# Kernel optimization log

Measured on AMD Instinct MI355X. Metric: run time of the kernel, lower is better.

Reference implementation:

```python
import jax, jax.numpy as jnp
import numpy as np

Z, Y, X = 16, 128, 128
B = 2
N_R, N_L = 12000, 20000   # active voxels per batch element (radar / lidar)
C = 64
IN_DIM = 4
NUM_LAYER = 2
K_LIST = (64, 32)         # knn fan-out = 64 / 2**layer
EPS = 1e-5


def _make_voxels(rng, n_per_batch):
    # unique voxel coords per batch, sorted by linear index (batch-major rows)
    out = []
    for b in range(B):
        lin = np.sort(rng.choice(Z * Y * X, size=n_per_batch, replace=False))
        z = lin // (Y * X); y = (lin // X) % Y; x = lin % X
        out.append(np.stack([np.full(n_per_batch, b), z, y, x], 1))
    return np.concatenate(out, 0).astype(np.int32)


def _nbr_map(coords):
    # 3x3x3 submanifold-conv rulebook: row index of each neighbor, -1 if absent
    b = coords[:, 0].astype(np.int64); z = coords[:, 1]; y = coords[:, 2]; x = coords[:, 3]
    keys = ((b * Z + z) * Y + y) * X + x  # globally sorted
    N = coords.shape[0]
    nbr = np.full((N, 27), -1, np.int64)
    k = 0
    for dz in (-1, 0, 1):
        for dy in (-1, 0, 1):
            for dx in (-1, 0, 1):
                nz, ny, nx = z + dz, y + dy, x + dx
                ok = (nz >= 0) & (nz < Z) & (ny >= 0) & (ny < Y) & (nx >= 0) & (nx < X)
                cand = ((b * Z + nz) * Y + ny) * X + nx
                pos = np.searchsorted(keys, cand)
                pos_c = np.clip(pos, 0, N - 1)
                hit = ok & (keys[pos_c] == cand)
                nbr[:, k] = np.where(hit, pos_c, -1)
                k += 1
    return nbr


def setup_inputs() -> dict:
    rng = np.random.default_rng(0)
    key = jax.random.key(0)
    ks = jax.random.split(key, 16)
    coordsR = _make_voxels(rng, N_R)
    coordsL = _make_voxels(rng, N_L)
    nbrR = _nbr_map(coordsR)
    nbrL = _nbr_map(coordsL)
    NLt = B * N_L
    # knn indices (global row ids into radar rows of same batch)
    knn0 = coordsL[:, 0:1].astype(np.int64) * N_R + rng.integers(0, N_R, (NLt, K_LIST[0]))
    knn1 = coordsL[:, 0:1].astype(np.int64) * N_R + rng.integers(0, N_R, (NLt, K_LIST[1]))
    sc = 1.0 / np.sqrt(27 * C).astype(np.float32)
    inp = {
        "featR": jax.random.normal(ks[0], (B * N_R, IN_DIM), jnp.float32),
        "featL": jax.random.normal(ks[1], (NLt, IN_DIM), jnp.float32),
        "img": jax.random.normal(ks[2], (B, 512), jnp.float32),
        "Win": jax.random.normal(ks[3], (2, IN_DIM, C), jnp.float32) * 0.1,
        "bin_": jnp.zeros((2, C), jnp.float32),
        # [layer, branch(R/L), conv(sp,subm_a,subm_b), 27, Cin, Cout]
        "Wconv": jax.random.normal(ks[4], (NUM_LAYER, 2, 3, 27, C, C), jnp.float32) * sc,
        "bconv": jnp.zeros((NUM_LAYER, 2, 3, C), jnp.float32),
        "bng": jnp.ones((NUM_LAYER, 2, 3, C), jnp.float32),
        "bnb": jnp.zeros((NUM_LAYER, 2, 3, C), jnp.float32),
        "Wimg": jax.random.normal(ks[5], (NUM_LAYER, 512, C), jnp.float32) * 0.05,
        "bimg": jnp.zeros((NUM_LAYER, C), jnp.float32),
        "Wval": jax.random.normal(ks[6], (NUM_LAYER, C, C), jnp.float32) * 0.125,
        "bval": jnp.zeros((NUM_LAYER, C), jnp.float32),
        "Wgate": jax.random.normal(ks[7], (NUM_LAYER, 2 * C, C), jnp.float32) * 0.09,
        "bgate": jnp.zeros((NUM_LAYER, C), jnp.float32),
        "Wbev": jax.random.normal(ks[8], (NUM_LAYER, 2, C * Z, C, 3, 3), jnp.float32) * (1.0 / np.sqrt(C * Z * 9).astype(np.float32)),
        "bbev": jnp.zeros((NUM_LAYER, 2, C), jnp.float32),
        "bntg": jnp.ones((NUM_LAYER, 2, C), jnp.float32),
        "bntb": jnp.zeros((NUM_LAYER, 2, C), jnp.float32),
        "nbrR": jnp.asarray(nbrR),
        "nbrL": jnp.asarray(nbrL),
        "knn0": jnp.asarray(knn0),
        "knn1": jnp.asarray(knn1),
        "coordsR": jnp.asarray(coordsR),
        "coordsL": jnp.asarray(coordsL),
    }
    return inp


def _bn1d(f, g, b):
    m = f.mean(0)
    v = f.var(0)
    return (f - m) / jnp.sqrt(v + EPS) * g + b


def _sconv(f, nbr, W, bias):
    # gather-scatter sparse 3D conv: out[n] = sum_k W[k] @ f[nbr[n,k]]
    mask = (nbr >= 0)[..., None].astype(f.dtype)
    g = f[jnp.clip(nbr, 0)] * mask                 # [N, 27, C]
    return jnp.einsum('nkc,kcd->nd', g, W) + bias


def _branch_block(f, nbr, Wc, bc, g, bt):
    # spconv -> bn -> relu, subm_a -> bn -> relu, subm_b -> bn -> relu
    for j in range(3):
        f = jax.nn.relu(_bn1d(_sconv(f, nbr, Wc[j], bc[j]), g[j], bt[j]))
    return f


def _to_bev(f, coords, Wt, bt, gg, gb):
    dense = jnp.zeros((B, Z, Y, X, C), f.dtype).at[
        coords[:, 0], coords[:, 1], coords[:, 2], coords[:, 3]].add(f)
    x2 = dense.transpose(0, 4, 1, 2, 3).reshape(B, C * Z, Y, X)  # 'b c z y x -> b (c z) y x'
    # ConvTranspose2d(k=3, s=1, p=1) == conv with swapped-IO, spatially flipped kernel, pad 1
    Wk = jnp.transpose(Wt, (1, 0, 2, 3))[:, :, ::-1, ::-1]
    out = jax.lax.conv_general_dilated(x2, Wk, (1, 1), ((1, 1), (1, 1)),
                                       dimension_numbers=('NCHW', 'OIHW', 'NCHW'))
    out = out + bt[:, None, None]
    m = out.mean((0, 2, 3), keepdims=True)
    v = out.var((0, 2, 3), keepdims=True)
    out = (out - m) / jnp.sqrt(v + EPS) * gg[:, None, None] + gb[:, None, None]
    return jax.nn.relu(out)


def reference(featR, featL, img, Win, bin_, Wconv, bconv, bng, bnb, Wimg, bimg,
              Wval, bval, Wgate, bgate, Wbev, bbev, bntg, bntb,
              nbrR, nbrL, knn0, knn1, coordsR, coordsL):
    fR = featR @ Win[0] + bin_[0]   # input_convR (1x1x1)
    fL = featL @ Win[1] + bin_[1]   # input_convL (1x1x1)
    knns = (knn0, knn1)
    bidL = coordsL[:, 0]
    bevs = []
    for l in range(NUM_LAYER):
        fR = _branch_block(fR, nbrR, Wconv[l, 0], bconv[l, 0], bng[l, 0], bnb[l, 0])
        fL = _branch_block(fL, nbrL, Wconv[l, 1], bconv[l, 1], bng[l, 1], bnb[l, 1])
        # knn cross-attention fusion: lidar queries K nearest radar voxels
        key = fR[knns[l]]                                        # [NL, K, C]
        val = jnp.einsum('nkc,cd->nkd', key, Wval[l]) + bval[l]
        attn = jax.nn.softmax(jnp.einsum('nc,nkc->nk', fL, key), axis=-1)
        fused = jnp.einsum('nk,nkd->nd', attn, val)
        imgf = jax.nn.sigmoid(img @ Wimg[l] + bimg[l])           # [B, C] weather condition
        fused = fused * imgf[bidL]
        gate = jax.nn.sigmoid(jnp.concatenate([fL, fused], -1) @ Wgate[l] + bgate[l])
        fL = fL + gate * fused
        bevs.append(_to_bev(fR, coordsR, Wbev[l, 0], bbev[l, 0], bntg[l, 0], bntb[l, 0]))
        bevs.append(_to_bev(fL, coordsL, Wbev[l, 1], bbev[l, 1], bntg[l, 1], bntb[l, 1]))
    return jnp.concatenate(bevs, axis=1)  # [B, 4*C, Y, X]
```

## Files before the change

kernel.cpp:

```cpp
#include <hip/hip_runtime.h>
#include <math.h>

#define NRT 24000
#define NLT 40000

static __device__ __forceinline__ float sigmoidf_(float x){ return 1.0f/(1.0f+expf(-x)); }

static __device__ __forceinline__ int xcd_swz(int bid, int nwg){
  int q = nwg>>3, r = nwg&7, x = bid&7, i = bid>>3;
  return (x<r ? x*(q+1) : r*(q+1)+(x-r)*q) + i;
}

__global__ void k_proj(const float* __restrict__ feat, const float* __restrict__ W,
                       const float* __restrict__ bias, float* __restrict__ out, int N){
  int i = blockIdx.x*256 + threadIdx.x;
  if (i >= N*64) return;
  int n = i >> 6, c = i & 63;
  const float* f = feat + n*4;
  out[i] = fmaf(f[0], W[c], fmaf(f[1], W[64+c], fmaf(f[2], W[128+c], fmaf(f[3], W[192+c], bias[c]))));
}

__global__ void k_kmask(const int* __restrict__ nbr, int NG, int* __restrict__ kmask){
  int g = blockIdx.x*64 + threadIdx.x;
  if (g >= NG) return;
  int m = 0;
  for (int v=0;v<4;v++){
    const int* row = nbr + (size_t)(g*4+v)*27;
    for (int k=0;k<27;k++) if (row[k] >= 0) m |= (1<<k);
  }
  kmask[g] = m;
}

__global__ void k_wc(const float* __restrict__ Wconv, float* __restrict__ WcT){
  int i = blockIdx.x*256+threadIdx.x;
  if (i >= 12*27*16*64*4) return;
  int j = i & 3; int r = i >> 2;
  int d = r & 63; r >>= 6;
  int c4 = r & 15; r >>= 4;
  int k = r % 27; int lc = r / 27;
  WcT[i] = Wconv[(size_t)lc*110592 + (size_t)k*4096 + (size_t)(4*c4+j)*64 + d];
}

__global__ void k_sconv(const float* __restrict__ fin, const int* __restrict__ nbr,
                        const int* __restrict__ kmask, const float* __restrict__ W,
                        float* __restrict__ fout, int N){
  int t = threadIdx.x & 63;
  int blk = xcd_swz(blockIdx.x, gridDim.x);
  int g = blk*4 + (threadIdx.x>>6);
  int n0 = g*4;
  float4 av[4];
  #pragma unroll
  for (int v=0;v<4;v++) av[v] = make_float4(0.f,0.f,0.f,0.f);
  const int* nrow = nbr + (size_t)n0*27;
  int m = kmask[g];
  while (m){
    int k = __builtin_ctz(m); m &= m-1;
    const float4* w4 = reinterpret_cast<const float4*>(W + (size_t)k*4096) + t;
    #pragma unroll
    for (int v=0;v<4;v++){
      int nb = nrow[27*v + k];
      if (nb >= 0){
        const float4* fr = reinterpret_cast<const float4*>(fin + (size_t)nb*64);
        float4 a = make_float4(0.f,0.f,0.f,0.f);
        #pragma unroll
        for (int c4=0;c4<16;c4++){
          float4 w = w4[c4*64];
          float4 f = fr[c4];
          a.x = fmaf(f.x, w.x, a.x);
          a.y = fmaf(f.y, w.y, a.y);
          a.z = fmaf(f.z, w.z, a.z);
          a.w = fmaf(f.w, w.w, a.w);
        }
        av[v].x += a.x; av[v].y += a.y; av[v].z += a.z; av[v].w += a.w;
      }
    }
  }
  #pragma unroll
  for (int v=0;v<4;v++)
    fout[(size_t)(n0+v)*64 + t] = (av[v].x+av[v].y)+(av[v].z+av[v].w);
}

__global__ void k_colsum(const float* __restrict__ f, int N, float* __restrict__ partial){
  int d = threadIdx.x & 63, sub = threadIdx.x >> 6;
  float s=0.f, s2=0.f;
  for (int n = blockIdx.x*4 + sub; n < N; n += 1024){
    float v = f[(size_t)n*64+d];
    s += v; s2 = fmaf(v,v,s2);
  }
  __shared__ float ls[4][64], ls2[4][64];
  ls[sub][d]=s; ls2[sub][d]=s2;
  __syncthreads();
  if (sub==0){
    s  = ls[0][d]+ls[1][d]+ls[2][d]+ls[3][d];
    s2 = ls2[0][d]+ls2[1][d]+ls2[2][d]+ls2[3][d];
    partial[(blockIdx.x*64+d)*2+0]=s;
    partial[(blockIdx.x*64+d)*2+1]=s2;
  }
}

__global__ void k_bnfin(const float* __restrict__ partial, int nblk, float invN,
                        const float* __restrict__ g, const float* __restrict__ b,
                        float* __restrict__ mv){
  int d = threadIdx.x;
  float s=0.f, s2=0.f;
  for (int i=0;i<nblk;i++){ s += partial[(i*64+d)*2]; s2 += partial[(i*64+d)*2+1]; }
  float mean = s*invN;
  float var  = s2*invN - mean*mean;
  float rstd = 1.0f/sqrtf(var + 1e-5f);
  float sc = g[d]*rstd;
  mv[d*2]   = sc;
  mv[d*2+1] = b[d] - mean*sc;
}

__global__ void k_bnrelu(float* __restrict__ f, const float* __restrict__ mv, int total){
  int i = blockIdx.x*256+threadIdx.x;
  if (i>=total) return;
  int c = i & 63;
  float v = fmaf(f[i], mv[c*2], mv[c*2+1]);
  f[i] = v>0.f? v:0.f;
}

__global__ void k_imgf(const float* __restrict__ img, const float* __restrict__ Wimg,
                       const float* __restrict__ bimg, float* __restrict__ imgf){
  int t = threadIdx.x;
  int b = t>>6, c = t&63;
  float s = bimg[c];
  const float* ir = img + b*512;
  for (int j=0;j<512;j++) s = fmaf(ir[j], Wimg[j*64+c], s);
  imgf[b*64+c] = sigmoidf_(s);
}

__global__ void k_attn(float* __restrict__ fL, const float* __restrict__ fR,
                       const int* __restrict__ knn, const int* __restrict__ coordsL,
                       const float* __restrict__ Wval, const float* __restrict__ bval,
                       const float* __restrict__ Wgate, const float* __restrict__ bgate,
                       const float* __restrict__ imgf, int K){
  __shared__ float keys[64*65];
  __shared__ float fls[64];
  __shared__ float aw[64];
  __shared__ float wks[64];
  __shared__ float fus[64];
  int n = blockIdx.x, t = threadIdx.x;
  float fl = fL[(size_t)n*64+t];
  fls[t] = fl;
  const int* kn = knn + (size_t)n*K;
  for (int k=0;k<K;k++){
    int r = kn[k];
    keys[k*65+t] = fR[(size_t)r*64+t];
  }
  __syncthreads();
  float s = -1e30f;
  if (t < K){
    const float* kr = keys + t*65;
    float a0 = 0.f;
    #pragma unroll
    for (int c=0;c<64;c++) a0 = fmaf(fls[c], kr[c], a0);
    s = a0;
  }
  float mx = s;
  #pragma unroll
  for (int m=32;m;m>>=1) mx = fmaxf(mx, __shfl_xor(mx, m, 64));
  float e = (t<K) ? expf(s-mx) : 0.f;
  float se = e;
  #pragma unroll
  for (int m=32;m;m>>=1) se += __shfl_xor(se, m, 64);
  aw[t] = e/se;
  __syncthreads();
  float wk = 0.f;
  for (int k=0;k<K;k++) wk = fmaf(aw[k], keys[k*65+t], wk);
  wks[t] = wk;
  __syncthreads();
  float fu = bval[t];
  #pragma unroll
  for (int c=0;c<64;c++) fu = fmaf(wks[c], Wval[c*64+t], fu);
  int bid = coordsL[n*4];
  fu *= imgf[bid*64+t];
  fus[t] = fu;
  __syncthreads();
  float gs = bgate[t];
  #pragma unroll
  for (int c=0;c<64;c++) gs = fmaf(fls[c], Wgate[c*64+t], gs);
  #pragma unroll
  for (int c=0;c<64;c++) gs = fmaf(fus[c], Wgate[(64+c)*64+t], gs);
  float gate = sigmoidf_(gs);
  fL[(size_t)n*64+t] = fl + gate*fu;
}

__global__ void k_grid(const int* __restrict__ coords, int N, int* __restrict__ grid){
  int n = blockIdx.x*256+threadIdx.x;
  if (n>=N) return;
  int b=coords[n*4], z=coords[n*4+1], y=coords[n*4+2], x=coords[n*4+3];
  grid[((b*128+y)*128+x)*16+z] = n;
}

__global__ void k_colbuild(const int* __restrict__ grid, int* __restrict__ ccnt,
                           int* __restrict__ cent){
  int col = blockIdx.x*256+threadIdx.x;
  if (col >= 2*128*128) return;
  const int* g = grid + col*16;
  int c=0;
  for (int z=0;z<16;z++){ int v=g[z]; if (v>=0) cent[col*16 + (c++)] = (v<<4)|z; }
  ccnt[col]=c;
}

__global__ void k_wt3(const float* __restrict__ Wbev, float* __restrict__ Wt3){
  int i = blockIdx.x*256+threadIdx.x;
  if (i >= 4*9*16*16*64*4) return;
  int j = i & 3; int r = i >> 2;
  int o = r & 63; r >>= 6;
  int c4 = r & 15; r >>= 4;
  int z = r & 15; r >>= 4;
  int q = r % 9; int ls = r / 9;
  int c = 4*c4 + j;
  int ky = 2-q/3, kx = 2-q%3;
  Wt3[i] = Wbev[(size_t)ls*589824 + (size_t)(c*16+z)*576 + o*9 + ky*3 + kx];
}

__global__ void k_bev(const float* __restrict__ f, const int* __restrict__ ccnt,
                      const int* __restrict__ cent, const float* __restrict__ Wt,
                      float* __restrict__ outp){
  int blk = xcd_swz(blockIdx.x, gridDim.x);
  int b = blk>>12; int rem = blk&4095; int y = rem>>5; int x0 = (rem&31)<<2;
  int t = threadIdx.x;
  float4 av[4];
  #pragma unroll
  for (int v=0;v<4;v++) av[v] = make_float4(0.f,0.f,0.f,0.f);
  #pragma unroll
  for (int dy=-1;dy<=1;dy++){
    int y2 = y+dy;
    if ((unsigned)y2 >= 128u) continue;
    int qb = (dy+1)*3;
    for (int cx=x0-1; cx<=x0+4; cx++){
      if ((unsigned)cx >= 128u) continue;
      int col = ((b<<7)+y2)*128 + cx;
      int cn = ccnt[col];
      const int* ce = cent + col*16;
      for (int i=0;i<cn;i++){
        int e = ce[i];
        int rid = e>>4, z = e&15;
        const float4* fr = reinterpret_cast<const float4*>(f + (size_t)rid*64);
        float4 fv[16];
        #pragma unroll
        for (int c4=0;c4<16;c4++) fv[c4] = fr[c4];
        #pragma unroll
        for (int v=0;v<4;v++){
          int dx = cx - (x0+v);
          if (dx>=-1 && dx<=1){
            int q = qb + dx + 1;
            const float4* w4 = reinterpret_cast<const float4*>(Wt + (size_t)(((q<<4)+z)<<12)) + t;
            float4 a = make_float4(0.f,0.f,0.f,0.f);
            #pragma unroll
            for (int c4=0;c4<16;c4++){
              float4 w = w4[c4*64];
              a.x = fmaf(fv[c4].x, w.x, a.x);
              a.y = fmaf(fv[c4].y, w.y, a.y);
              a.z = fmaf(fv[c4].z, w.z, a.z);
              a.w = fmaf(fv[c4].w, w.w, a.w);
            }
            av[v].x += a.x; av[v].y += a.y; av[v].z += a.z; av[v].w += a.w;
          }
        }
      }
    }
  }
  float4 o4;
  o4.x = (av[0].x+av[0].y)+(av[0].z+av[0].w);
  o4.y = (av[1].x+av[1].y)+(av[1].z+av[1].w);
  o4.z = (av[2].x+av[2].y)+(av[2].z+av[2].w);
  o4.w = (av[3].x+av[3].y)+(av[3].z+av[3].w);
  *reinterpret_cast<float4*>(outp + (size_t)b*(256*16384) + (size_t)t*16384 + y*128 + x0) = o4;
}

__global__ void k_bevstat(const float* __restrict__ outp, const float* __restrict__ g,
                          const float* __restrict__ b, float* __restrict__ mv){
  int ch = blockIdx.x, t = threadIdx.x;
  float s=0.f, s2=0.f;
  for (int bb=0;bb<2;bb++){
    const float* base = outp + (size_t)bb*(256*16384) + (size_t)ch*16384;
    for (int p=t;p<16384;p+=256){ float v = base[p]; s+=v; s2=fmaf(v,v,s2); }
  }
  __shared__ float ls[256], ls2[256];
  ls[t]=s; ls2[t]=s2; __syncthreads();
  for (int m=128;m;m>>=1){ if (t<m){ ls[t]+=ls[t+m]; ls2[t]+=ls2[t+m]; } __syncthreads(); }
  if (t==0){
    float mean = ls[0]*(1.0f/32768.0f);
    float var  = ls2[0]*(1.0f/32768.0f) - mean*mean;
    float rstd = 1.0f/sqrtf(var+1e-5f);
    float sc = g[ch]*rstd;
    mv[ch*2]=sc; mv[ch*2+1]=b[ch]-mean*sc;
  }
}

__global__ void k_bevbn(float* __restrict__ outp, const float* __restrict__ mv){
  int i = blockIdx.x*256+threadIdx.x;
  if (i >= 2*64*16384) return;
  int bb = i>>20; int r = i & ((1<<20)-1);
  int ch = r>>14; int p = r&16383;
  float* a = outp + (size_t)bb*(256*16384) + (size_t)ch*16384 + p;
  float v = fmaf(*a, mv[ch*2], mv[ch*2+1]);
  *a = v>0.f? v:0.f;
}

extern "C" void kernel_launch(void* const* d_in, const int* in_sizes, int n_in,
                              void* d_out, int out_size, void* d_ws, size_t ws_size,
                              hipStream_t stream){
  const float* featR = (const float*)d_in[0];
  const float* featL = (const float*)d_in[1];
  const float* img   = (const float*)d_in[2];
  const float* Win   = (const float*)d_in[3];
  const float* bin_  = (const float*)d_in[4];
  const float* Wconv = (const float*)d_in[5];
  const float* bng   = (const float*)d_in[7];
  const float* bnb   = (const float*)d_in[8];
  const float* Wimg  = (const float*)d_in[9];
  const float* bimg  = (const float*)d_in[10];
  const float* Wval  = (const float*)d_in[11];
  const float* bval  = (const float*)d_in[12];
  const float* Wgate = (const float*)d_in[13];
  const float* bgate = (const float*)d_in[14];
  const float* Wbev  = (const float*)d_in[15];
  const float* bntg  = (const float*)d_in[17];
  const float* bntb  = (const float*)d_in[18];
  const int* nbrR    = (const int*)d_in[19];
  const int* nbrL    = (const int*)d_in[20];
  const int* knn0    = (const int*)d_in[21];
  const int* knn1    = (const int*)d_in[22];
  const int* coordsR = (const int*)d_in[23];
  const int* coordsL = (const int*)d_in[24];
  float* outp = (float*)d_out;

  char* w = (char*)d_ws;
  auto alloc = [&](size_t bytes){ char* p = w; w += (bytes + 255) & ~(size_t)255; return p; };
  float* fRa = (float*)alloc((size_t)NRT*64*4);
  float* fRb = (float*)alloc((size_t)NRT*64*4);
  float* fLa = (float*)alloc((size_t)NLT*64*4);
  float* fLb = (float*)alloc((size_t)NLT*64*4);
  int*   gridR = (int*)alloc((size_t)2*128*128*16*4);
  int*   gridL = (int*)alloc((size_t)2*128*128*16*4);
  float* Wt3 = (float*)alloc((size_t)4*9*16*16*64*4*4);
  float* WcT = (float*)alloc((size_t)12*27*16*64*4*4);
  float* imgfbuf = (float*)alloc(2*64*4);
  float* partial = (float*)alloc((size_t)256*64*2*4);
  float* mv = (float*)alloc(64*2*4);
  int* kmaskR = (int*)alloc((size_t)(NRT/4)*4);
  int* kmaskL = (int*)alloc((size_t)(NLT/4)*4);
  int* ccntR = (int*)alloc((size_t)2*128*128*4);
  int* ccntL = (int*)alloc((size_t)2*128*128*4);
  int* centR = (int*)alloc((size_t)2*128*128*16*4);
  int* centL = (int*)alloc((size_t)2*128*128*16*4);

  hipMemsetAsync(gridR, 0xFF, (size_t)2*128*128*16*4, stream);
  hipMemsetAsync(gridL, 0xFF, (size_t)2*128*128*16*4, stream);
  k_grid<<<(NRT+255)/256,256,0,stream>>>(coordsR, NRT, gridR);
  k_grid<<<(NLT+255)/256,256,0,stream>>>(coordsL, NLT, gridL);
  k_colbuild<<<(2*128*128+255)/256,256,0,stream>>>(gridR, ccntR, centR);
  k_colbuild<<<(2*128*128+255)/256,256,0,stream>>>(gridL, ccntL, centL);
  k_kmask<<<((NRT/4)+63)/64,64,0,stream>>>(nbrR, NRT/4, kmaskR);
  k_kmask<<<((NLT/4)+63)/64,64,0,stream>>>(nbrL, NLT/4, kmaskL);
  k_wt3<<<(4*9*16*16*64*4+255)/256,256,0,stream>>>(Wbev, Wt3);
  k_wc<<<(12*27*16*64*4+255)/256,256,0,stream>>>(Wconv, WcT);

  k_proj<<<(NRT*64+255)/256,256,0,stream>>>(featR, Win,     bin_,    fRa, NRT);
  k_proj<<<(NLT*64+255)/256,256,0,stream>>>(featL, Win+256, bin_+64, fLa, NLT);

  float* fRcur=fRa; float* fRalt=fRb; float* fLcur=fLa; float* fLalt=fLb;
  for (int l=0;l<2;l++){
    for (int j=0;j<3;j++){
      const float* Wc = WcT + (size_t)((l*2+0)*3+j)*110592;
      k_sconv<<<NRT/16,256,0,stream>>>(fRcur, nbrR, kmaskR, Wc, fRalt, NRT);
      k_colsum<<<256,256,0,stream>>>(fRalt, NRT, partial);
      k_bnfin<<<1,64,0,stream>>>(partial, 256, 1.0f/NRT,
                                 bng + ((l*2+0)*3+j)*64, bnb + ((l*2+0)*3+j)*64, mv);
      k_bnrelu<<<(NRT*64+255)/256,256,0,stream>>>(fRalt, mv, NRT*64);
      float* tmp=fRcur; fRcur=fRalt; fRalt=tmp;
    }
    for (int j=0;j<3;j++){
      const float* Wc = WcT + (size_t)((l*2+1)*3+j)*110592;
      k_sconv<<<NLT/16,256,0,stream>>>(fLcur, nbrL, kmaskL, Wc, fLalt, NLT);
      k_colsum<<<256,256,0,stream>>>(fLalt, NLT, partial);
      k_bnfin<<<1,64,0,stream>>>(partial, 256, 1.0f/NLT,
                                 bng + ((l*2+1)*3+j)*64, bnb + ((l*2+1)*3+j)*64, mv);
      k_bnrelu<<<(NLT*64+255)/256,256,0,stream>>>(fLalt, mv, NLT*64);
      float* tmp=fLcur; fLcur=fLalt; fLalt=tmp;
    }
    k_imgf<<<1,128,0,stream>>>(img, Wimg + (size_t)l*512*64, bimg + l*64, imgfbuf);
    const int* knn = (l==0)? knn0 : knn1;
    int K = (l==0)? 64 : 32;
    k_attn<<<NLT,64,0,stream>>>(fLcur, fRcur, knn, coordsL,
                                Wval + (size_t)l*4096, bval + l*64,
                                Wgate + (size_t)l*8192, bgate + l*64,
                                imgfbuf, K);
    {
      float* op = outp + (size_t)(2*l)*64*16384;
      const float* wt = Wt3 + (size_t)(l*2+0)*9*16*4096;
      k_bev<<<2*128*32,64,0,stream>>>(fRcur, ccntR, centR, wt, op);
      k_bevstat<<<64,256,0,stream>>>(op, bntg + (l*2+0)*64, bntb + (l*2+0)*64, mv);
      k_bevbn<<<(2*64*16384+255)/256,256,0,stream>>>(op, mv);
    }
    {
      float* op = outp + (size_t)(2*l+1)*64*16384;
      const float* wt = Wt3 + (size_t)(l*2+1)*9*16*4096;
      k_bev<<<2*128*32,64,0,stream>>>(fLcur, ccntL, centL, wt, op);
      k_bevstat<<<64,256,0,stream>>>(op, bntg + (l*2+1)*64, bntb + (l*2+1)*64, mv);
      k_bevbn<<<(2*64*16384+255)/256,256,0,stream>>>(op, mv);
    }
  }
}
```

Measured before the change: 3.225 ms.

## Hoist conv weights into registers and split BEV conv into gather-GEMM plus scatter

```diff
diff --git a/kernel.cpp b/kernel.cpp
--- a/kernel.cpp
+++ b/kernel.cpp
@@ -20,12 +20,12 @@
   out[i] = fmaf(f[0], W[c], fmaf(f[1], W[64+c], fmaf(f[2], W[128+c], fmaf(f[3], W[192+c], bias[c]))));
 }
 
-__global__ void k_kmask(const int* __restrict__ nbr, int NG, int* __restrict__ kmask){
+__global__ void k_kmask16(const int* __restrict__ nbr, int NG, int* __restrict__ kmask){
   int g = blockIdx.x*64 + threadIdx.x;
   if (g >= NG) return;
   int m = 0;
-  for (int v=0;v<4;v++){
-    const int* row = nbr + (size_t)(g*4+v)*27;
+  for (int v=0;v<16;v++){
+    const int* row = nbr + (size_t)(g*16+v)*27;
     for (int k=0;k<27;k++) if (row[k] >= 0) m |= (1<<k);
   }
   kmask[g] = m;
@@ -47,37 +47,38 @@
   int t = threadIdx.x & 63;
   int blk = xcd_swz(blockIdx.x, gridDim.x);
   int g = blk*4 + (threadIdx.x>>6);
-  int n0 = g*4;
-  float4 av[4];
-  #pragma unroll
-  for (int v=0;v<4;v++) av[v] = make_float4(0.f,0.f,0.f,0.f);
+  int n0 = g*16;
+  float acc[16];
+  #pragma unroll
+  for (int v=0;v<16;v++) acc[v] = 0.f;
   const int* nrow = nbr + (size_t)n0*27;
   int m = kmask[g];
   while (m){
     int k = __builtin_ctz(m); m &= m-1;
-    const float4* w4 = reinterpret_cast<const float4*>(W + (size_t)k*4096) + t;
+    const float4* w4 = reinterpret_cast<const float4*>(W) + k*1024 + t;
+    float4 wreg[16];
     #pragma unroll
-    for (int v=0;v<4;v++){
+    for (int c4=0;c4<16;c4++) wreg[c4] = w4[c4*64];
+    #pragma unroll
+    for (int v=0;v<16;v++){
       int nb = nrow[27*v + k];
       if (nb >= 0){
         const float4* fr = reinterpret_cast<const float4*>(fin + (size_t)nb*64);
         float4 a = make_float4(0.f,0.f,0.f,0.f);
         #pragma unroll
         for (int c4=0;c4<16;c4++){
-          float4 w = w4[c4*64];
-          float4 f = fr[c4];
-          a.x = fmaf(f.x, w.x, a.x);
-          a.y = fmaf(f.y, w.y, a.y);
-          a.z = fmaf(f.z, w.z, a.z);
-          a.w = fmaf(f.w, w.w, a.w);
+          float4 fv = fr[c4];
+          a.x = fmaf(fv.x, wreg[c4].x, a.x);
+          a.y = fmaf(fv.y, wreg[c4].y, a.y);
+          a.z = fmaf(fv.z, wreg[c4].z, a.z);
+          a.w = fmaf(fv.w, wreg[c4].w, a.w);
         }
-        av[v].x += a.x; av[v].y += a.y; av[v].z += a.z; av[v].w += a.w;
+        acc[v] += (a.x+a.y)+(a.z+a.w);
       }
     }
   }
   #pragma unroll
-  for (int v=0;v<4;v++)
-    fout[(size_t)(n0+v)*64 + t] = (av[v].x+av[v].y)+(av[v].z+av[v].w);
+  for (int v=0;v<16;v++) fout[(size_t)(n0+v)*64 + t] = acc[v];
 }
 
 __global__ void k_colsum(const float* __restrict__ f, int N, float* __restrict__ partial){
@@ -203,6 +204,15 @@
   ccnt[col]=c;
 }
 
+__global__ void k_zlist(const int* __restrict__ coords, int N, int* __restrict__ zcnt,
+                        int* __restrict__ zlist, int zcap){
+  int n = blockIdx.x*256+threadIdx.x;
+  if (n>=N) return;
+  int z = coords[n*4+1];
+  int slot = atomicAdd(&zcnt[z], 1);
+  zlist[z*zcap + slot] = n;
+}
+
 __global__ void k_wt3(const float* __restrict__ Wbev, float* __restrict__ Wt3){
   int i = blockIdx.x*256+threadIdx.x;
   if (i >= 4*9*16*16*64*4) return;
@@ -216,58 +226,64 @@
   Wt3[i] = Wbev[(size_t)ls*589824 + (size_t)(c*16+z)*576 + o*9 + ky*3 + kx];
 }
 
-__global__ void k_bev(const float* __restrict__ f, const int* __restrict__ ccnt,
-                      const int* __restrict__ cent, const float* __restrict__ Wt,
-                      float* __restrict__ outp){
+__global__ void k_bevg(const float* __restrict__ f, const int* __restrict__ zcnt,
+                       const int* __restrict__ zlist, int zcap,
+                       const float* __restrict__ Wt,
+                       float* __restrict__ tmp, int CH){
+  int task = blockIdx.x / CH, chunk = blockIdx.x % CH;
+  int q = task >> 4, z = task & 15;
+  int t = threadIdx.x;
+  const float4* w4 = reinterpret_cast<const float4*>(Wt + (size_t)(((q<<4)+z)<<12)) + t;
+  float4 wreg[16];
+  #pragma unroll
+  for (int c4=0;c4<16;c4++) wreg[c4] = w4[c4*64];
+  int cnt = zcnt[z];
+  const int* zl = zlist + z*zcap;
+  for (int i=chunk; i<cnt; i+=CH){
+    int v = zl[i];
+    const float4* fr = reinterpret_cast<const float4*>(f + (size_t)v*64);
+    float4 a = make_float4(0.f,0.f,0.f,0.f);
+    #pragma unroll
+    for (int c4=0;c4<16;c4++){
+      float4 fv = fr[c4];
+      a.x = fmaf(fv.x, wreg[c4].x, a.x);
+      a.y = fmaf(fv.y, wreg[c4].y, a.y);
+      a.z = fmaf(fv.z, wreg[c4].z, a.z);
+      a.w = fmaf(fv.w, wreg[c4].w, a.w);
+    }
+    tmp[((size_t)v*9+q)*64 + t] = (a.x+a.y)+(a.z+a.w);
+  }
+}
+
+__global__ void k_bevs(const float* __restrict__ tmp, const int* __restrict__ ccnt,
+                       const int* __restrict__ cent, float* __restrict__ outp){
   int blk = xcd_swz(blockIdx.x, gridDim.x);
   int b = blk>>12; int rem = blk&4095; int y = rem>>5; int x0 = (rem&31)<<2;
   int t = threadIdx.x;
-  float4 av[4];
-  #pragma unroll
-  for (int v=0;v<4;v++) av[v] = make_float4(0.f,0.f,0.f,0.f);
+  float acc[4] = {0.f,0.f,0.f,0.f};
   #pragma unroll
   for (int dy=-1;dy<=1;dy++){
     int y2 = y+dy;
     if ((unsigned)y2 >= 128u) continue;
-    int qb = (dy+1)*3;
+    int qb = (dy+1)*3 + 1;
     for (int cx=x0-1; cx<=x0+4; cx++){
       if ((unsigned)cx >= 128u) continue;
       int col = ((b<<7)+y2)*128 + cx;
       int cn = ccnt[col];
       const int* ce = cent + col*16;
+      int d0 = cx - x0;
       for (int i=0;i<cn;i++){
-        int e = ce[i];
-        int rid = e>>4, z = e&15;
-        const float4* fr = reinterpret_cast<const float4*>(f + (size_t)rid*64);
-        float4 fv[16];
-        #pragma unroll
-        for (int c4=0;c4<16;c4++) fv[c4] = fr[c4];
+        int rid = ce[i]>>4;
+        const float* tb = tmp + (size_t)rid*576 + qb*64 + t;
         #pragma unroll
         for (int v=0;v<4;v++){
-          int dx = cx - (x0+v);
-          if (dx>=-1 && dx<=1){
-            int q = qb + dx + 1;
-            const float4* w4 = reinterpret_cast<const float4*>(Wt + (size_t)(((q<<4)+z)<<12)) + t;
-            float4 a = make_float4(0.f,0.f,0.f,0.f);
-            #pragma unroll
-            for (int c4=0;c4<16;c4++){
-              float4 w = w4[c4*64];
-              a.x = fmaf(fv[c4].x, w.x, a.x);
-              a.y = fmaf(fv[c4].y, w.y, a.y);
-              a.z = fmaf(fv[c4].z, w.z, a.z);
-              a.w = fmaf(fv[c4].w, w.w, a.w);
-            }
-            av[v].x += a.x; av[v].y += a.y; av[v].z += a.z; av[v].w += a.w;
-          }
+          int dx = d0 - v;
+          if (dx>=-1 && dx<=1) acc[v] += tb[dx*64];
         }
       }
     }
   }
-  float4 o4;
-  o4.x = (av[0].x+av[0].y)+(av[0].z+av[0].w);
-  o4.y = (av[1].x+av[1].y)+(av[1].z+av[1].w);
-  o4.z = (av[2].x+av[2].y)+(av[2].z+av[2].w);
-  o4.w = (av[3].x+av[3].y)+(av[3].z+av[3].w);
+  float4 o4 = make_float4(acc[0],acc[1],acc[2],acc[3]);
   *reinterpret_cast<float4*>(outp + (size_t)b*(256*16384) + (size_t)t*16384 + y*128 + x0) = o4;
 }
 
@@ -342,46 +358,54 @@
   float* imgfbuf = (float*)alloc(2*64*4);
   float* partial = (float*)alloc((size_t)256*64*2*4);
   float* mv = (float*)alloc(64*2*4);
-  int* kmaskR = (int*)alloc((size_t)(NRT/4)*4);
-  int* kmaskL = (int*)alloc((size_t)(NLT/4)*4);
+  int* kmaskR = (int*)alloc((size_t)(NRT/16)*4);
+  int* kmaskL = (int*)alloc((size_t)(NLT/16)*4);
   int* ccntR = (int*)alloc((size_t)2*128*128*4);
   int* ccntL = (int*)alloc((size_t)2*128*128*4);
   int* centR = (int*)alloc((size_t)2*128*128*16*4);
   int* centL = (int*)alloc((size_t)2*128*128*16*4);
+  int* zcnt  = (int*)alloc(32*4);
+  int* zlistR = (int*)alloc((size_t)16*NRT*4);
+  int* zlistL = (int*)alloc((size_t)16*NLT*4);
+  float* tmp = (float*)alloc((size_t)NLT*576*4);
 
   hipMemsetAsync(gridR, 0xFF, (size_t)2*128*128*16*4, stream);
   hipMemsetAsync(gridL, 0xFF, (size_t)2*128*128*16*4, stream);
+  hipMemsetAsync(zcnt, 0, 32*4, stream);
   k_grid<<<(NRT+255)/256,256,0,stream>>>(coordsR, NRT, gridR);
   k_grid<<<(NLT+255)/256,256,0,stream>>>(coordsL, NLT, gridL);
   k_colbuild<<<(2*128*128+255)/256,256,0,stream>>>(gridR, ccntR, centR);
   k_colbuild<<<(2*128*128+255)/256,256,0,stream>>>(gridL, ccntL, centL);
-  k_kmask<<<((NRT/4)+63)/64,64,0,stream>>>(nbrR, NRT/4, kmaskR);
-  k_kmask<<<((NLT/4)+63)/64,64,0,stream>>>(nbrL, NLT/4, kmaskL);
+  k_zlist<<<(NRT+255)/256,256,0,stream>>>(coordsR, NRT, zcnt,    zlistR, NRT);
+  k_zlist<<<(NLT+255)/256,256,0,stream>>>(coordsL, NLT, zcnt+16, zlistL, NLT);
+  k_kmask16<<<((NRT/16)+63)/64,64,0,stream>>>(nbrR, NRT/16, kmaskR);
+  k_kmask16<<<((NLT/16)+63)/64,64,0,stream>>>(nbrL, NLT/16, kmaskL);
   k_wt3<<<(4*9*16*16*64*4+255)/256,256,0,stream>>>(Wbev, Wt3);
   k_wc<<<(12*27*16*64*4+255)/256,256,0,stream>>>(Wconv, WcT);
 
   k_proj<<<(NRT*64+255)/256,256,0,stream>>>(featR, Win,     bin_,    fRa, NRT);
   k_proj<<<(NLT*64+255)/256,256,0,stream>>>(featL, Win+256, bin_+64, fLa, NLT);
 
+  const int CH = 32;
   float* fRcur=fRa; float* fRalt=fRb; float* fLcur=fLa; float* fLalt=fLb;
   for (int l=0;l<2;l++){
     for (int j=0;j<3;j++){
       const float* Wc = WcT + (size_t)((l*2+0)*3+j)*110592;
-      k_sconv<<<NRT/16,256,0,stream>>>(fRcur, nbrR, kmaskR, Wc, fRalt, NRT);
+      k_sconv<<<NRT/64,256,0,stream>>>(fRcur, nbrR, kmaskR, Wc, fRalt, NRT);
       k_colsum<<<256,256,0,stream>>>(fRalt, NRT, partial);
       k_bnfin<<<1,64,0,stream>>>(partial, 256, 1.0f/NRT,
                                  bng + ((l*2+0)*3+j)*64, bnb + ((l*2+0)*3+j)*64, mv);
       k_bnrelu<<<(NRT*64+255)/256,256,0,stream>>>(fRalt, mv, NRT*64);
-      float* tmp=fRcur; fRcur=fRalt; fRalt=tmp;
+      float* tmpp=fRcur; fRcur=fRalt; fRalt=tmpp;
     }
     for (int j=0;j<3;j++){
       const float* Wc = WcT + (size_t)((l*2+1)*3+j)*110592;
-      k_sconv<<<NLT/16,256,0,stream>>>(fLcur, nbrL, kmaskL, Wc, fLalt, NLT);
+      k_sconv<<<NLT/64,256,0,stream>>>(fLcur, nbrL, kmaskL, Wc, fLalt, NLT);
       k_colsum<<<256,256,0,stream>>>(fLalt, NLT, partial);
       k_bnfin<<<1,64,0,stream>>>(partial, 256, 1.0f/NLT,
                                  bng + ((l*2+1)*3+j)*64, bnb + ((l*2+1)*3+j)*64, mv);
       k_bnrelu<<<(NLT*64+255)/256,256,0,stream>>>(fLalt, mv, NLT*64);
-      float* tmp=fLcur; fLcur=fLalt; fLalt=tmp;
+      float* tmpp=fLcur; fLcur=fLalt; fLalt=tmpp;
     }
     k_imgf<<<1,128,0,stream>>>(img, Wimg + (size_t)l*512*64, bimg + l*64, imgfbuf);
     const int* knn = (l==0)? knn0 : knn1;
@@ -392,15 +416,17 @@
                                 imgfbuf, K);
     {
       float* op = outp + (size_t)(2*l)*64*16384;
-      const float* wt = Wt3 + (size_t)(l*2+0)*9*16*4096;
-      k_bev<<<2*128*32,64,0,stream>>>(fRcur, ccntR, centR, wt, op);
+      const float* wt = Wt3 + (size_t)(l*2+0)*589824;
+      k_bevg<<<144*CH,64,0,stream>>>(fRcur, zcnt,    zlistR, NRT, wt, tmp, CH);
+      k_bevs<<<2*128*32,64,0,stream>>>(tmp, ccntR, centR, op);
       k_bevstat<<<64,256,0,stream>>>(op, bntg + (l*2+0)*64, bntb + (l*2+0)*64, mv);
       k_bevbn<<<(2*64*16384+255)/256,256,0,stream>>>(op, mv);
     }
     {
       float* op = outp + (size_t)(2*l+1)*64*16384;
-      const float* wt = Wt3 + (size_t)(l*2+1)*9*16*4096;
-      k_bev<<<2*128*32,64,0,stream>>>(fLcur, ccntL, centL, wt, op);
+      const float* wt = Wt3 + (size_t)(l*2+1)*589824;
+      k_bevg<<<144*CH,64,0,stream>>>(fLcur, zcnt+16, zlistL, NLT, wt, tmp, CH);
+      k_bevs<<<2*128*32,64,0,stream>>>(tmp, ccntL, centL, op);
       k_bevstat<<<64,256,0,stream>>>(op, bntg + (l*2+1)*64, bntb + (l*2+1)*64, mv);
       k_bevbn<<<(2*64*16384+255)/256,256,0,stream>>>(op, mv);
     }
```

Result: slower. 4.383 ms (+35.9%).
